# Performance work log

Hardware: AMD Instinct MI355X
Metric: run time of the kernel (lower is better)

Reference implementation:

```python
import jax, jax.numpy as jnp
import numpy as np

B, N, D = 2, 2048, 1024
CTX, TV = 256, 250
H, DH = 16, 64
INNER = H * DH          # 1024
FF = 4 * D              # 4096 (GEGLU inner)
SCALE = DH ** -0.5


def _layernorm(x, g, b):
    mu = x.mean(-1, keepdims=True)
    var = ((x - mu) ** 2).mean(-1, keepdims=True)
    return (x - mu) / jnp.sqrt(var + 1e-5) * g + b


def _attn(xq, ctx, wq, wk, wv, wo, bo):
    b, n, _ = xq.shape
    m = ctx.shape[1]
    q = (xq @ wq).reshape(b, n, H, DH)
    k = (ctx @ wk).reshape(b, m, H, DH)
    v = (ctx @ wv).reshape(b, m, H, DH)
    sim = jnp.einsum('bihd,bjhd->bhij', q, k) * SCALE
    att = jax.nn.softmax(sim, axis=-1)
    out = jnp.einsum('bhij,bjhd->bihd', att, v).reshape(b, n, INNER)
    return out @ wo + bo


def _sin_pe(T, d):
    pos = jnp.arange(T, dtype=jnp.float32)[:, None]
    den = jnp.power(10000.0, 2.0 * jnp.arange(d // 2, dtype=jnp.float32) / d)
    ang = pos / den                                  # [T, d/2]
    return jnp.stack([jnp.sin(ang), jnp.cos(ang)], -1).reshape(T, d)


def setup_inputs() -> dict:
    key = jax.random.key(0)
    ks = jax.random.split(key, 40)
    w = lambda k, s: jax.random.normal(k, s, jnp.float32) * 0.02
    inp = {
        'x': jax.random.normal(ks[0], (B, N, D), jnp.float32),
        'context': jax.random.normal(ks[1], (B, CTX, D), jnp.float32),
        'hint_control': jax.random.normal(ks[2], (B, TV, D), jnp.float32),
        'ln1_g': jnp.ones((D,)), 'ln1_b': jnp.zeros((D,)),
        'ln2_g': jnp.ones((D,)), 'ln2_b': jnp.zeros((D,)),
        'ln3_g': jnp.ones((D,)), 'ln3_b': jnp.zeros((D,)),
        'ln4_g': jnp.ones((D,)), 'ln4_b': jnp.zeros((D,)),
        'a1_wq': w(ks[3], (D, INNER)), 'a1_wk': w(ks[4], (D, INNER)),
        'a1_wv': w(ks[5], (D, INNER)), 'a1_wo': w(ks[6], (INNER, D)),
        'a1_bo': jnp.zeros((D,)),
        'a2_wq': w(ks[7], (D, INNER)), 'a2_wk': w(ks[8], (D, INNER)),
        'a2_wv': w(ks[9], (D, INNER)), 'a2_wo': w(ks[10], (INNER, D)),
        'a2_bo': jnp.zeros((D,)),
        'a3_wq': w(ks[11], (D, INNER)), 'a3_wk': w(ks[12], (D, INNER)),
        'a3_wv': w(ks[13], (D, INNER)), 'a3_wo': w(ks[14], (INNER, D)),
        'a3_bo': jnp.zeros((D,)),
        'ff_w1': w(ks[15], (D, 2 * FF)), 'ff_b1': jnp.zeros((2 * FF,)),
        'ff_w2': w(ks[16], (FF, D)), 'ff_b2': jnp.zeros((D,)),
    }
    return inp


def reference(x, context, hint_control,
              ln1_g, ln1_b, ln2_g, ln2_b, ln3_g, ln3_b, ln4_g, ln4_b,
              a1_wq, a1_wk, a1_wv, a1_wo, a1_bo,
              a2_wq, a2_wk, a2_wv, a2_wo, a2_bo,
              a3_wq, a3_wk, a3_wv, a3_wo, a3_bo,
              ff_w1, ff_b1, ff_w2, ff_b2):
    # attn1: self-attention (disable_self_attn=False -> context is x itself)
    h = _layernorm(x, ln1_g, ln1_b)
    x = _attn(h, h, a1_wq, a1_wk, a1_wv, a1_wo, a1_bo) + x
    # attn2: cross-attention over context
    h = _layernorm(x, ln2_g, ln2_b)
    x = _attn(h, context, a2_wq, a2_wk, a2_wv, a2_wo, a2_bo) + x
    # attn3: video cross-attention with sinusoidal PE added to hint_control
    hint = hint_control + _sin_pe(hint_control.shape[1], D)[None]
    h = _layernorm(x, ln4_g, ln4_b)
    x = _attn(h, hint, a3_wq, a3_wk, a3_wv, a3_wo, a3_bo) + x
    # GEGLU feed-forward
    h = _layernorm(x, ln3_g, ln3_b)
    proj = h @ ff_w1 + ff_b1
    a, gate = jnp.split(proj, 2, axis=-1)
    x = (a * jax.nn.gelu(gate, approximate=False)) @ ff_w2 + ff_b2 + x
    return x
```

## Files before the change

kernel.cpp:

```cpp
#include <hip/hip_runtime.h>
#include <cstdint>

typedef unsigned short u16;
typedef __bf16 bf16x8 __attribute__((ext_vector_type(8)));
typedef float f32x4 __attribute__((ext_vector_type(4)));

__device__ __forceinline__ u16 f2bf(float f) {
  union { float f; uint32_t u; } x; x.f = f;
  uint32_t r = x.u + 0x7FFFu + ((x.u >> 16) & 1u);
  return (u16)(r >> 16);
}
__device__ __forceinline__ bf16x8 ld8s(const u16* p) {
  return *reinterpret_cast<const bf16x8*>(p);
}
__device__ __forceinline__ float geluf(float x) {
  return 0.5f * x * (1.f + erff(x * 0.70710678118654752f));
}
__device__ __forceinline__ uint32_t cvtpk(float a, float b) {
  uint32_t r;
  asm("v_cvt_pk_bf16_f32 %0, %1, %2" : "=v"(r) : "v"(a), "v"(b));
  return r;
}
__device__ __forceinline__ void gload16(const u16* g, u16* l) {
  __builtin_amdgcn_global_load_lds(
      (__attribute__((address_space(1))) void*)const_cast<u16*>(g),
      (__attribute__((address_space(3))) void*)l, 16, 0, 0);
}

struct PrepJob {
  const void* src; void* dst;
  int K, N, mode, row_off, ldo, s_lo, s_hi, blk0;
};
struct PrepArgs { PrepJob j[17]; };

__global__ __launch_bounds__(256) void wprep_kernel(PrepArgs a) {
  __shared__ float tile[32][33];
  int bid = blockIdx.x;
  int t = threadIdx.x;
  const float* src = nullptr; void* dst = nullptr;
  int K = 0, N = 0, mode = 0, roff = 0, ldo = 0, slo = 0, shi = 0, bl = 0;
#pragma unroll
  for (int i = 0; i < 17; ++i) {
    int lo = a.j[i].blk0;
    int hi = (i == 16) ? 0x7fffffff : a.j[i + 1].blk0;
    if (bid >= lo && bid < hi) {
      src = (const float*)a.j[i].src; dst = a.j[i].dst;
      K = a.j[i].K; N = a.j[i].N; mode = a.j[i].mode; roff = a.j[i].row_off;
      ldo = a.j[i].ldo; slo = a.j[i].s_lo; shi = a.j[i].s_hi; bl = bid - lo;
    }
  }
  (void)K;
  if (mode <= 1) {
    int nb = N >> 5;
    int bx = bl % nb, by = bl / nb;
    int tx = t & 31, ty = t >> 5;
    int n = bx * 32 + tx, kbase = by * 32;
#pragma unroll
    for (int r = 0; r < 4; ++r)
      tile[ty + r * 8][tx] = src[(size_t)(kbase + ty + r * 8) * N + n];
    __syncthreads();
#pragma unroll
    for (int r = 0; r < 4; ++r) {
      int nl = ty + r * 8, ng = bx * 32 + nl;
      int orow;
      if (mode == 0) orow = roff + ng;
      else {
        if (ng < 4096) orow = ((ng >> 4) << 5) + (ng & 15);
        else { int t2 = ng - 4096; orow = ((t2 >> 4) << 5) + 16 + (t2 & 15); }
      }
      float v = tile[tx][nl];
      if (mode == 0 && orow >= slo && orow < shi) v *= 0.18033688011112042f;
      ((u16*)dst)[(size_t)orow * ldo + kbase + tx] = f2bf(v);
    }
  } else if (mode == 2) {
    int idx = bl * 1024 + t * 4;
    float4 v = *reinterpret_cast<const float4*>(src + idx);
    ushort4 o;
    o.x = f2bf(v.x); o.y = f2bf(v.y); o.z = f2bf(v.z); o.w = f2bf(v.w);
    *reinterpret_cast<ushort4*>((u16*)dst + idx) = o;
  } else if (mode == 3) {
    int row = bl;
    int tt = row % 250;
    int d0 = t * 4;
    int i0 = d0 >> 1;
    float den0 = powf(10000.f, (float)i0 / 512.f);
    float den1 = powf(10000.f, (float)(i0 + 1) / 512.f);
    float a0 = (float)tt / den0, a1 = (float)tt / den1;
    const float* hp = src + (size_t)row * 1024 + d0;
    u16* op = (u16*)dst + (size_t)row * 1024 + d0;
    op[0] = f2bf(hp[0] + sinf(a0));
    op[1] = f2bf(hp[1] + cosf(a0));
    op[2] = f2bf(hp[2] + sinf(a1));
    op[3] = f2bf(hp[3] + cosf(a1));
  } else {
    int i2 = bl * 256 + t;
    int g = i2 >> 5, s2 = i2 & 31;
    int c2 = (s2 < 16) ? (g * 16 + s2) : (4096 + g * 16 + (s2 - 16));
    ((float*)dst)[i2] = src[c2];
  }
}

__global__ __launch_bounds__(256) void ln_kernel(const float* __restrict__ x,
                                                 const float* __restrict__ g,
                                                 const float* __restrict__ b,
                                                 u16* __restrict__ out) {
  int row = blockIdx.x;
  int tid = threadIdx.x;
  int l = tid & 63, w = tid >> 6;
  const float4 v = reinterpret_cast<const float4*>(x + (size_t)row * 1024)[tid];
  float s = v.x + v.y + v.z + v.w;
#pragma unroll
  for (int d = 1; d < 64; d <<= 1) s += __shfl_xor(s, d, 64);
  __shared__ float red[8];
  if (l == 0) red[w] = s;
  __syncthreads();
  float mean = (red[0] + red[1] + red[2] + red[3]) * (1.f / 1024.f);
  float dx = v.x - mean, dy = v.y - mean, dz = v.z - mean, dw = v.w - mean;
  float vs = dx * dx + dy * dy + dz * dz + dw * dw;
#pragma unroll
  for (int d = 1; d < 64; d <<= 1) vs += __shfl_xor(vs, d, 64);
  if (l == 0) red[4 + w] = vs;
  __syncthreads();
  float var = (red[4] + red[5] + red[6] + red[7]) * (1.f / 1024.f);
  float rstd = rsqrtf(var + 1e-5f);
  const float4 g4 = reinterpret_cast<const float4*>(g)[tid];
  const float4 b4 = reinterpret_cast<const float4*>(b)[tid];
  ushort4 o;
  o.x = f2bf(dx * rstd * g4.x + b4.x);
  o.y = f2bf(dy * rstd * g4.y + b4.y);
  o.z = f2bf(dz * rstd * g4.z + b4.z);
  o.w = f2bf(dw * rstd * g4.w + b4.w);
  reinterpret_cast<ushort4*>(out + (size_t)row * 1024)[tid] = o;
}

template <int EPI>
__global__ __launch_bounds__(512, 2) void gemm256_kernel(
    const u16* __restrict__ A, int lda, const u16* __restrict__ Bt,
    void* __restrict__ Cv, int ldc, const float* __restrict__ bias,
    int M, int N, int K) {
  __shared__ __align__(16) u16 As[2][256 * 64];
  __shared__ __align__(16) u16 Bs[2][256 * 64];
  int t = threadIdx.x;
  int l = t & 63, w = t >> 6;
  int wm = w >> 2, wn = w & 3;
  int lr = l & 15, lg = l >> 4;
  int gx = gridDim.x;
  int nwg = gx * gridDim.y;
  int orig = blockIdx.y * gx + blockIdx.x;
  int qq = nwg >> 3, rr = nwg & 7;
  int xcd = orig & 7, lin = orig >> 3;
  int wg = (xcd < rr ? xcd * (qq + 1) : rr * (qq + 1) + (xcd - rr) * qq) + lin;
  int bx = wg % gx, by = wg / gx;
  int row0 = by * 256, n0 = bx * 256;

  int lrow8 = l >> 3, lchunk = l & 7;
  int csrc = (lchunk ^ lrow8) * 8;
  int keyA = lr & 15 & 7;
  int c0 = ((lg ^ keyA) << 3);
  int c1 = (((4 + lg) ^ keyA) << 3);

  f32x4 acc[8][4];
#pragma unroll
  for (int i = 0; i < 8; ++i)
#pragma unroll
    for (int j = 0; j < 4; ++j) acc[i][j] = f32x4{0.f, 0.f, 0.f, 0.f};

  auto stA = [&](int buf, int k0, int q) {
    int rb = q * 64 + w * 8;
    gload16(&A[(size_t)(row0 + rb + lrow8) * lda + k0 + csrc], &As[buf][rb * 64]);
  };
  auto stB = [&](int buf, int k0, int q) {
    int rb = q * 64 + w * 8;
    gload16(&Bt[(size_t)(n0 + rb + lrow8) * K + k0 + csrc], &Bs[buf][rb * 64]);
  };

  int nk = K >> 6;
  stB(0, 0, 0); stB(0, 0, 1); stB(0, 0, 2); stB(0, 0, 3);
  stA(0, 0, 0); stA(0, 0, 2); stA(0, 0, 1); stA(0, 0, 3);
  asm volatile("s_waitcnt vmcnt(2)" ::: "memory");
  __builtin_amdgcn_sched_barrier(0);
  asm volatile("s_barrier" ::: "memory");

  for (int ti = 0; ti < nk; ++ti) {
    int cur = ti & 1, nxt = cur ^ 1;
    bool hn = (ti + 1 < nk);
    int k0n = (ti + 1) << 6;
    const u16* Ab = As[cur];
    const u16* Bb = Bs[cur];
    bf16x8 a[4], b[4];

#pragma unroll
    for (int mi = 0; mi < 4; ++mi) a[mi] = ld8s(&Ab[(wm * 128 + mi * 16 + lr) * 64 + c0]);
#pragma unroll
    for (int ni = 0; ni < 4; ++ni) b[ni] = ld8s(&Bb[(wn * 64 + ni * 16 + lr) * 64 + c0]);
    if (hn) { stB(nxt, k0n, 0); stB(nxt, k0n, 1); }
    asm volatile("s_barrier" ::: "memory");
    __builtin_amdgcn_s_setprio(1);
#pragma unroll
    for (int mi = 0; mi < 4; ++mi)
#pragma unroll
      for (int ni = 0; ni < 4; ++ni)
        acc[mi][ni] = __builtin_amdgcn_mfma_f32_16x16x32_bf16(a[mi], b[ni], acc[mi][ni], 0, 0, 0);
    __builtin_amdgcn_s_setprio(0);
    if (hn) asm volatile("s_waitcnt vmcnt(2)" ::: "memory");
    else    asm volatile("s_waitcnt vmcnt(0)" ::: "memory");
    __builtin_amdgcn_sched_barrier(0);
    asm volatile("s_barrier" ::: "memory");

#pragma unroll
    for (int mi = 0; mi < 4; ++mi) a[mi] = ld8s(&Ab[(wm * 128 + (mi + 4) * 16 + lr) * 64 + c0]);
    if (hn) { stB(nxt, k0n, 2); stB(nxt, k0n, 3); }
    asm volatile("s_barrier" ::: "memory");
    __builtin_amdgcn_s_setprio(1);
#pragma unroll
    for (int mi = 0; mi < 4; ++mi)
#pragma unroll
      for (int ni = 0; ni < 4; ++ni)
        acc[mi + 4][ni] = __builtin_amdgcn_mfma_f32_16x16x32_bf16(a[mi], b[ni], acc[mi + 4][ni], 0, 0, 0);
    __builtin_amdgcn_s_setprio(0);
    asm volatile("s_barrier" ::: "memory");

#pragma unroll
    for (int mi = 0; mi < 4; ++mi) a[mi] = ld8s(&Ab[(wm * 128 + mi * 16 + lr) * 64 + c1]);
#pragma unroll
    for (int ni = 0; ni < 4; ++ni) b[ni] = ld8s(&Bb[(wn * 64 + ni * 16 + lr) * 64 + c1]);
    if (hn) { stA(nxt, k0n, 0); stA(nxt, k0n, 2); }
    asm volatile("s_barrier" ::: "memory");
    __builtin_amdgcn_s_setprio(1);
#pragma unroll
    for (int mi = 0; mi < 4; ++mi)
#pragma unroll
      for (int ni = 0; ni < 4; ++ni)
        acc[mi][ni] = __builtin_amdgcn_mfma_f32_16x16x32_bf16(a[mi], b[ni], acc[mi][ni], 0, 0, 0);
    __builtin_amdgcn_s_setprio(0);
    asm volatile("s_barrier" ::: "memory");

#pragma unroll
    for (int mi = 0; mi < 4; ++mi) a[mi] = ld8s(&Ab[(wm * 128 + (mi + 4) * 16 + lr) * 64 + c1]);
    if (hn) { stA(nxt, k0n, 1); stA(nxt, k0n, 3); }
    asm volatile("s_barrier" ::: "memory");
    __builtin_amdgcn_s_setprio(1);
#pragma unroll
    for (int mi = 0; mi < 4; ++mi)
#pragma unroll
      for (int ni = 0; ni < 4; ++ni)
        acc[mi + 4][ni] = __builtin_amdgcn_mfma_f32_16x16x32_bf16(a[mi], b[ni], acc[mi + 4][ni], 0, 0, 0);
    __builtin_amdgcn_s_setprio(0);
    if (hn) asm volatile("s_waitcnt vmcnt(2)" ::: "memory");
    __builtin_amdgcn_sched_barrier(0);
    asm volatile("s_barrier" ::: "memory");
  }

#pragma unroll
  for (int mi = 0; mi < 8; ++mi) {
    int rowb = row0 + wm * 128 + mi * 16 + lg * 4;
    if (EPI == 2) {
#pragma unroll
      for (int p = 0; p < 2; ++p) {
        int colA = n0 + wn * 64 + p * 32 + lr;
        int colG = colA + 16;
        int ocol = ((n0 + wn * 64) >> 1) + p * 16 + lr;
#pragma unroll
        for (int r = 0; r < 4; ++r) {
          float av = acc[mi][2 * p][r] + bias[colA];
          float gv = acc[mi][2 * p + 1][r] + bias[colG];
          ((u16*)Cv)[(size_t)(rowb + r) * ldc + ocol] = f2bf(av * geluf(gv));
        }
      }
    } else {
#pragma unroll
      for (int ni = 0; ni < 4; ++ni) {
        int gcol = n0 + wn * 64 + ni * 16 + lr;
#pragma unroll
        for (int r = 0; r < 4; ++r)
          ((u16*)Cv)[(size_t)(rowb + r) * ldc + gcol] = f2bf(acc[mi][ni][r]);
      }
    }
  }
}

template <int EPI, bool GUARD>
__global__ __launch_bounds__(256) void gemm_bt_kernel(
    const u16* __restrict__ A, int lda, const u16* __restrict__ Bt,
    void* __restrict__ Cv, int ldc, const float* __restrict__ bias,
    const float* __restrict__ res, int M, int N, int K) {
  __shared__ __align__(16) u16 As[2][128 * 64];
  __shared__ __align__(16) u16 Bs[2][128 * 64];
  int t = threadIdx.x;
  int l = t & 63, w = t >> 6;
  int wm = w >> 1, wn = w & 1;
  int lr = l & 15, lg = l >> 4;
  int gx = gridDim.x;
  int nwg = gx * gridDim.y;
  int orig = blockIdx.y * gx + blockIdx.x;
  int qq = nwg >> 3, rr = nwg & 7;
  int xcd = orig & 7, lin = orig >> 3;
  int wg = (xcd < rr ? xcd * (qq + 1) : rr * (qq + 1) + (xcd - rr) * qq) + lin;
  int bx = wg % gx, by = wg / gx;
  int row0 = by * 128, n0 = bx * 128;

  int lrow8 = l >> 3, lchunk = l & 7;
  int csrc = (lchunk ^ lrow8) * 8;
  int keyA = lr & 7;
  f32x4 acc[4][4];
#pragma unroll
  for (int i = 0; i < 4; ++i)
#pragma unroll
    for (int j = 0; j < 4; ++j) acc[i][j] = f32x4{0.f, 0.f, 0.f, 0.f};

  auto stage = [&](int buf, int k0) {
#pragma unroll
    for (int q = 0; q < 4; ++q) {
      int rbase = w * 32 + q * 8;
      int r = rbase + lrow8;
      int ga = row0 + r;
      if (GUARD) { if (ga > M - 1) ga = M - 1; }
      gload16(&A[(size_t)ga * lda + k0 + csrc], &As[buf][rbase * 64]);
      gload16(&Bt[(size_t)(n0 + r) * K + k0 + csrc], &Bs[buf][rbase * 64]);
    }
  };

  int nk = K >> 6;
  stage(0, 0);
  if (nk > 1) {
    stage(1, 64);
    asm volatile("s_waitcnt vmcnt(8)" ::: "memory");
  } else {
    asm volatile("s_waitcnt vmcnt(0)" ::: "memory");
  }
  __builtin_amdgcn_sched_barrier(0);
  __builtin_amdgcn_s_barrier();
  int cur = 0;
  for (int ti = 0; ti < nk; ++ti) {
    __builtin_amdgcn_s_setprio(1);
#pragma unroll
    for (int kk = 0; kk < 2; ++kk) {
      bf16x8 af[4], bfv[4];
#pragma unroll
      for (int mi = 0; mi < 4; ++mi)
        af[mi] = ld8s(&As[cur][(wm * 64 + mi * 16 + lr) * 64 + ((((kk << 2) + lg) ^ keyA) << 3)]);
#pragma unroll
      for (int ni = 0; ni < 4; ++ni)
        bfv[ni] = ld8s(&Bs[cur][(wn * 64 + ni * 16 + lr) * 64 + ((((kk << 2) + lg) ^ keyA) << 3)]);
#pragma unroll
      for (int mi = 0; mi < 4; ++mi)
#pragma unroll
        for (int ni = 0; ni < 4; ++ni)
          acc[mi][ni] = __builtin_amdgcn_mfma_f32_16x16x32_bf16(af[mi], bfv[ni], acc[mi][ni], 0, 0, 0);
    }
    __builtin_amdgcn_s_setprio(0);
    __builtin_amdgcn_sched_barrier(0);
    __builtin_amdgcn_s_barrier();
    if (ti + 2 < nk) {
      stage(cur, (ti + 2) << 6);
      asm volatile("s_waitcnt vmcnt(8)" ::: "memory");
    } else {
      asm volatile("s_waitcnt vmcnt(0)" ::: "memory");
    }
    __builtin_amdgcn_sched_barrier(0);
    __builtin_amdgcn_s_barrier();
    cur ^= 1;
  }

#pragma unroll
  for (int mi = 0; mi < 4; ++mi) {
    int rowb = row0 + wm * 64 + mi * 16 + lg * 4;
    if (EPI == 2) {
#pragma unroll
      for (int p = 0; p < 2; ++p) {
        int colA = n0 + wn * 64 + p * 32 + lr;
        int colG = colA + 16;
        int ocol = ((n0 + wn * 64) >> 1) + p * 16 + lr;
#pragma unroll
        for (int r = 0; r < 4; ++r) {
          int grow = rowb + r;
          float av = acc[mi][2 * p][r] + bias[colA];
          float gv = acc[mi][2 * p + 1][r] + bias[colG];
          ((u16*)Cv)[(size_t)grow * ldc + ocol] = f2bf(av * geluf(gv));
        }
      }
    } else {
#pragma unroll
      for (int ni = 0; ni < 4; ++ni) {
        int gcol = n0 + wn * 64 + ni * 16 + lr;
#pragma unroll
        for (int r = 0; r < 4; ++r) {
          int grow = rowb + r;
          if (GUARD && grow >= M) continue;
          float v = acc[mi][ni][r];
          if (EPI == 0)
            ((u16*)Cv)[(size_t)grow * ldc + gcol] = f2bf(v);
          else
            ((float*)Cv)[(size_t)grow * ldc + gcol] =
                v + bias[gcol] + res[(size_t)grow * ldc + gcol];
        }
      }
    }
  }
}

template <bool TG>
__global__ __launch_bounds__(256) void attn_kernel(
    const u16* __restrict__ Q, int qs, int qoff,
    const u16* __restrict__ KV, int kvs, int koff, int voff,
    int m, u16* __restrict__ O) {
  int b = blockIdx.z, h = blockIdx.y;
  int t = threadIdx.x;
  int l = t & 63, w = t >> 6;
  int lr = l & 15, lg = l >> 4;
  int q0 = blockIdx.x * 128 + w * 16;
  __shared__ __align__(16) u16 Ks[2][64 * 64];
  __shared__ __align__(16) u16 Vt[2][64 * 64];
  __shared__ __align__(16) u16 Pl[4][16 * 64];

  const u16* qrowA = Q + (size_t)((b << 11) + q0 + lr) * qs + qoff + h * 64;
  const u16* qrowB = qrowA + (size_t)64 * qs;
  bf16x8 qa0 = ld8s(qrowA + lg * 8), qa1 = ld8s(qrowA + 32 + lg * 8);
  bf16x8 qb0 = ld8s(qrowB + lg * 8), qb1 = ld8s(qrowB + 32 + lg * 8);

  f32x4 oA[4], oB[4];
  float psA = 0.f, psB = 0.f;
#pragma unroll
  for (int r = 0; r < 4; ++r) { oA[r] = f32x4{0.f, 0.f, 0.f, 0.f}; oB[r] = f32x4{0.f, 0.f, 0.f, 0.f}; }

  const u16* kvb = KV + (size_t)b * m * kvs + h * 64;
  int kj = t >> 3, kc = t & 7;
  int srcsw = ((l & 7) ^ (l >> 3)) << 3;
  int psw = (lr & 7) ^ ((lr & 8) >> 1);

  {
#pragma unroll
    for (int q2 = 0; q2 < 2; ++q2) {
      int gr = w * 16 + q2 * 8 + (l >> 3);
      if (TG) { if (gr > m - 1) gr = m - 1; }
      gload16(kvb + (size_t)gr * kvs + koff + srcsw, &Ks[0][(w * 16 + q2 * 8) * 64]);
    }
    int jv = kj * 2;
    int gv0 = jv, gv1 = jv + 1;
    if (TG) { if (gv0 > m - 1) gv0 = m - 1; if (gv1 > m - 1) gv1 = m - 1; }
    uint4 va = *reinterpret_cast<const uint4*>(kvb + (size_t)gv0 * kvs + voff + kc * 8);
    uint4 vb2 = *reinterpret_cast<const uint4*>(kvb + (size_t)gv1 * kvs + voff + kc * 8);
    const u16* vap = reinterpret_cast<const u16*>(&va);
    const u16* vbp = reinterpret_cast<const u16*>(&vb2);
    int jb = jv >> 3, jlow = jv & 7;
#pragma unroll
    for (int i = 0; i < 8; ++i) {
      int d = kc * 8 + i;
      int key = (d ^ (d >> 3)) & 7;
      uint32_t pk = (uint32_t)vap[i] | ((uint32_t)vbp[i] << 16);
      *reinterpret_cast<uint32_t*>(&Vt[0][d * 64 + ((jb ^ key) << 3) + jlow]) = pk;
    }
  }
  __syncthreads();

  int nj = (m + 63) >> 6;
  int cur = 0;
  for (int jt = 0; jt < nj; ++jt) {
    int j0 = jt << 6;
    bool hn = (jt + 1 < nj);
    uint4 va, vb2;
    if (hn) {
      int j0n = j0 + 64;
#pragma unroll
      for (int q2 = 0; q2 < 2; ++q2) {
        int gr = j0n + w * 16 + q2 * 8 + (l >> 3);
        if (TG) { if (gr > m - 1) gr = m - 1; }
        gload16(kvb + (size_t)gr * kvs + koff + srcsw, &Ks[cur ^ 1][(w * 16 + q2 * 8) * 64]);
      }
      int jv = kj * 2;
      int gv0 = j0n + jv, gv1 = j0n + jv + 1;
      if (TG) { if (gv0 > m - 1) gv0 = m - 1; if (gv1 > m - 1) gv1 = m - 1; }
      va = *reinterpret_cast<const uint4*>(kvb + (size_t)gv0 * kvs + voff + kc * 8);
      vb2 = *reinterpret_cast<const uint4*>(kvb + (size_t)gv1 * kvs + voff + kc * 8);
    }

    const u16* Kb = Ks[cur];
    f32x4 sA[4], sB[4];
#pragma unroll
    for (int c = 0; c < 4; ++c) {
      sA[c] = f32x4{0.f, 0.f, 0.f, 0.f};
      sB[c] = f32x4{0.f, 0.f, 0.f, 0.f};
      bf16x8 k0 = ld8s(&Kb[(c * 16 + lr) * 64 + ((lg ^ (lr & 7)) << 3)]);
      bf16x8 k1 = ld8s(&Kb[(c * 16 + lr) * 64 + (((4 + lg) ^ (lr & 7)) << 3)]);
      sA[c] = __builtin_amdgcn_mfma_f32_16x16x32_bf16(k0, qa0, sA[c], 0, 0, 0);
      sA[c] = __builtin_amdgcn_mfma_f32_16x16x32_bf16(k1, qa1, sA[c], 0, 0, 0);
      sB[c] = __builtin_amdgcn_mfma_f32_16x16x32_bf16(k0, qb0, sB[c], 0, 0, 0);
      sB[c] = __builtin_amdgcn_mfma_f32_16x16x32_bf16(k1, qb1, sB[c], 0, 0, 0);
    }

    if (hn) {
      const u16* vap = reinterpret_cast<const u16*>(&va);
      const u16* vbp = reinterpret_cast<const u16*>(&vb2);
      int jv = kj * 2;
      int jb = jv >> 3, jlow = jv & 7;
#pragma unroll
      for (int i = 0; i < 8; ++i) {
        int d = kc * 8 + i;
        int key = (d ^ (d >> 3)) & 7;
        uint32_t pk = (uint32_t)vap[i] | ((uint32_t)vbp[i] << 16);
        *reinterpret_cast<uint32_t*>(&Vt[cur ^ 1][d * 64 + ((jb ^ key) << 3) + jlow]) = pk;
      }
    }

    bool tail = TG && (j0 + 64 > m);
    const u16* Vb = Vt[cur];
    bf16x8 vfr[2][4];

    {
      uint32_t pk[8];
#pragma unroll
      for (int c = 0; c < 4; ++c) {
        float p[4];
#pragma unroll
        for (int r = 0; r < 4; ++r) {
          float v = exp2f(sA[c][r]);
          if (tail && (j0 + c * 16 + lg * 4 + r >= m)) v = 0.f;
          p[r] = v; psA += v;
        }
        pk[2 * c] = cvtpk(p[0], p[1]);
        pk[2 * c + 1] = cvtpk(p[2], p[3]);
      }
#pragma unroll
      for (int c = 0; c < 4; ++c) {
        int phys = (2 * c + (lg >> 1)) ^ psw;
        uint2 u; u.x = pk[2 * c]; u.y = pk[2 * c + 1];
        *reinterpret_cast<uint2*>(&Pl[w][lr * 64 + (phys << 3) + ((lg & 1) << 2)]) = u;
      }
#pragma unroll
      for (int ks = 0; ks < 2; ++ks) {
        int physp = (ks * 4 + lg) ^ psw;
        bf16x8 pb = ld8s(&Pl[w][lr * 64 + (physp << 3)]);
#pragma unroll
        for (int dt = 0; dt < 4; ++dt) {
          int d = dt * 16 + lr;
          int key = (d ^ (d >> 3)) & 7;
          vfr[ks][dt] = ld8s(&Vb[d * 64 + ((((ks << 2) + lg) ^ key) << 3)]);
          oA[dt] = __builtin_amdgcn_mfma_f32_16x16x32_bf16(vfr[ks][dt], pb, oA[dt], 0, 0, 0);
        }
      }
    }
    {
      uint32_t pk[8];
#pragma unroll
      for (int c = 0; c < 4; ++c) {
        float p[4];
#pragma unroll
        for (int r = 0; r < 4; ++r) {
          float v = exp2f(sB[c][r]);
          if (tail && (j0 + c * 16 + lg * 4 + r >= m)) v = 0.f;
          p[r] = v; psB += v;
        }
        pk[2 * c] = cvtpk(p[0], p[1]);
        pk[2 * c + 1] = cvtpk(p[2], p[3]);
      }
#pragma unroll
      for (int c = 0; c < 4; ++c) {
        int phys = (2 * c + (lg >> 1)) ^ psw;
        uint2 u; u.x = pk[2 * c]; u.y = pk[2 * c + 1];
        *reinterpret_cast<uint2*>(&Pl[w][lr * 64 + (phys << 3) + ((lg & 1) << 2)]) = u;
      }
#pragma unroll
      for (int ks = 0; ks < 2; ++ks) {
        int physp = (ks * 4 + lg) ^ psw;
        bf16x8 pb = ld8s(&Pl[w][lr * 64 + (physp << 3)]);
#pragma unroll
        for (int dt = 0; dt < 4; ++dt)
          oB[dt] = __builtin_amdgcn_mfma_f32_16x16x32_bf16(vfr[ks][dt], pb, oB[dt], 0, 0, 0);
      }
    }
    __syncthreads();
    cur ^= 1;
  }

  psA += __shfl_xor(psA, 16, 64); psA += __shfl_xor(psA, 32, 64);
  psB += __shfl_xor(psB, 16, 64); psB += __shfl_xor(psB, 32, 64);
  float invA = 1.f / psA, invB = 1.f / psB;
  {
    int grow = (b << 11) + q0 + lr;
    u16* op = O + (size_t)grow * 1024 + h * 64 + lg * 4;
#pragma unroll
    for (int dt = 0; dt < 4; ++dt) {
      uint2 u;
      u.x = cvtpk(oA[dt][0] * invA, oA[dt][1] * invA);
      u.y = cvtpk(oA[dt][2] * invA, oA[dt][3] * invA);
      *reinterpret_cast<uint2*>(op + dt * 16) = u;
    }
    u16* op2 = op + (size_t)64 * 1024;
#pragma unroll
    for (int dt = 0; dt < 4; ++dt) {
      uint2 u;
      u.x = cvtpk(oB[dt][0] * invB, oB[dt][1] * invB);
      u.y = cvtpk(oB[dt][2] * invB, oB[dt][3] * invB);
      *reinterpret_cast<uint2*>(op2 + dt * 16) = u;
    }
  }
}

extern "C" void kernel_launch(void* const* d_in, const int* in_sizes, int n_in,
                              void* d_out, int out_size, void* d_ws, size_t ws_size,
                              hipStream_t stream) {
  const float* x_in = (const float*)d_in[0];
  const float* ctx_in = (const float*)d_in[1];
  const float* hint_in = (const float*)d_in[2];
  const float* ln1g = (const float*)d_in[3]; const float* ln1b = (const float*)d_in[4];
  const float* ln2g = (const float*)d_in[5]; const float* ln2b = (const float*)d_in[6];
  const float* ln3g = (const float*)d_in[7]; const float* ln3b = (const float*)d_in[8];
  const float* ln4g = (const float*)d_in[9]; const float* ln4b = (const float*)d_in[10];
  const float* a1wq = (const float*)d_in[11]; const float* a1wk = (const float*)d_in[12];
  const float* a1wv = (const float*)d_in[13]; const float* a1wo = (const float*)d_in[14];
  const float* a1bo = (const float*)d_in[15];
  const float* a2wq = (const float*)d_in[16]; const float* a2wk = (const float*)d_in[17];
  const float* a2wv = (const float*)d_in[18]; const float* a2wo = (const float*)d_in[19];
  const float* a2bo = (const float*)d_in[20];
  const float* a3wq = (const float*)d_in[21]; const float* a3wk = (const float*)d_in[22];
  const float* a3wv = (const float*)d_in[23]; const float* a3wo = (const float*)d_in[24];
  const float* a3bo = (const float*)d_in[25];
  const float* ffw1 = (const float*)d_in[26]; const float* ffb1 = (const float*)d_in[27];
  const float* ffw2 = (const float*)d_in[28]; const float* ffb2 = (const float*)d_in[29];

  char* wsb = (char*)d_ws;
  size_t off = 0;
  auto alloc = [&](size_t bytes) -> void* {
    void* p = wsb + off;
    off += (bytes + 255) & ~(size_t)255;
    return p;
  };
  u16* wqkv1t = (u16*)alloc(3072ull * 1024 * 2);
  u16* wo1t = (u16*)alloc(1024ull * 1024 * 2);
  u16* wq2t = (u16*)alloc(1024ull * 1024 * 2);
  u16* wkv2t = (u16*)alloc(2048ull * 1024 * 2);
  u16* wo2t = (u16*)alloc(1024ull * 1024 * 2);
  u16* wq3t = (u16*)alloc(1024ull * 1024 * 2);
  u16* wkv3t = (u16*)alloc(2048ull * 1024 * 2);
  u16* wo3t = (u16*)alloc(1024ull * 1024 * 2);
  u16* w1t = (u16*)alloc(8192ull * 1024 * 2);
  u16* w2t = (u16*)alloc(1024ull * 4096 * 2);
  float* b1p = (float*)alloc(8192ull * 4);
  u16* hintbf = (u16*)alloc(500ull * 1024 * 2);
  u16* ctxbf = (u16*)alloc(512ull * 1024 * 2);
  float* xbuf = (float*)alloc(4096ull * 1024 * 4);
  u16* hbf = (u16*)alloc(4096ull * 1024 * 2);
  u16* attnout = (u16*)alloc(4096ull * 1024 * 2);
  u16* qbuf = (u16*)alloc(4096ull * 1024 * 2);
  u16* kvbuf = (u16*)alloc(512ull * 2048 * 2);
  u16* qkv = (u16*)alloc(4096ull * 4096 * 2);
  u16* gbuf = qkv;

  PrepArgs pa;
  int bi = 0, bc = 0;
  auto addJ = [&](const void* s, void* d, int K, int N, int mode, int roff,
                  int ldo, int slo, int shi, int nblk) {
    pa.j[bi].src = s; pa.j[bi].dst = d; pa.j[bi].K = K; pa.j[bi].N = N;
    pa.j[bi].mode = mode; pa.j[bi].row_off = roff; pa.j[bi].ldo = ldo;
    pa.j[bi].s_lo = slo; pa.j[bi].s_hi = shi; pa.j[bi].blk0 = bc;
    bc += nblk; ++bi;
  };
  addJ(a1wq, wqkv1t, 1024, 1024, 0, 0, 1024, 0, 1024, 1024);
  addJ(a1wk, wqkv1t, 1024, 1024, 0, 1024, 1024, 0, 0, 1024);
  addJ(a1wv, wqkv1t, 1024, 1024, 0, 2048, 1024, 0, 0, 1024);
  addJ(a1wo, wo1t, 1024, 1024, 0, 0, 1024, 0, 0, 1024);
  addJ(a2wq, wq2t, 1024, 1024, 0, 0, 1024, 0, 1024, 1024);
  addJ(a2wk, wkv2t, 1024, 1024, 0, 0, 1024, 0, 0, 1024);
  addJ(a2wv, wkv2t, 1024, 1024, 0, 1024, 1024, 0, 0, 1024);
  addJ(a2wo, wo2t, 1024, 1024, 0, 0, 1024, 0, 0, 1024);
  addJ(a3wq, wq3t, 1024, 1024, 0, 0, 1024, 0, 1024, 1024);
  addJ(a3wk, wkv3t, 1024, 1024, 0, 0, 1024, 0, 0, 1024);
  addJ(a3wv, wkv3t, 1024, 1024, 0, 1024, 1024, 0, 0, 1024);
  addJ(a3wo, wo3t, 1024, 1024, 0, 0, 1024, 0, 0, 1024);
  addJ(ffw1, w1t, 1024, 8192, 1, 0, 1024, 0, 0, 8192);
  addJ(ffw2, w2t, 4096, 1024, 0, 0, 4096, 0, 0, 4096);
  addJ(ctx_in, ctxbf, 0, 0, 2, 0, 0, 0, 0, 512);
  addJ(hint_in, hintbf, 0, 0, 3, 0, 0, 0, 0, 500);
  addJ(ffb1, b1p, 0, 0, 4, 0, 0, 0, 0, 32);
  wprep_kernel<<<bc, 256, 0, stream>>>(pa);

  ln_kernel<<<4096, 256, 0, stream>>>(x_in, ln1g, ln1b, hbf);
  gemm256_kernel<0><<<dim3(12, 16), 512, 0, stream>>>(hbf, 1024, wqkv1t, qkv, 3072,
                                                      nullptr, 4096, 3072, 1024);
  attn_kernel<false><<<dim3(16, 16, 2), 256, 0, stream>>>(qkv, 3072, 0, qkv, 3072, 1024, 2048,
                                                          2048, attnout);
  gemm_bt_kernel<1, false><<<dim3(8, 32), 256, 0, stream>>>(attnout, 1024, wo1t, xbuf, 1024,
                                                            a1bo, x_in, 4096, 1024, 1024);

  ln_kernel<<<4096, 256, 0, stream>>>(xbuf, ln2g, ln2b, hbf);
  gemm_bt_kernel<0, false><<<dim3(8, 32), 256, 0, stream>>>(hbf, 1024, wq2t, qbuf, 1024,
                                                            nullptr, nullptr, 4096, 1024, 1024);
  gemm_bt_kernel<0, false><<<dim3(16, 4), 256, 0, stream>>>(ctxbf, 1024, wkv2t, kvbuf, 2048,
                                                            nullptr, nullptr, 512, 2048, 1024);
  attn_kernel<false><<<dim3(16, 16, 2), 256, 0, stream>>>(qbuf, 1024, 0, kvbuf, 2048, 0, 1024,
                                                          256, attnout);
  gemm_bt_kernel<1, false><<<dim3(8, 32), 256, 0, stream>>>(attnout, 1024, wo2t, xbuf, 1024,
                                                            a2bo, xbuf, 4096, 1024, 1024);

  ln_kernel<<<4096, 256, 0, stream>>>(xbuf, ln4g, ln4b, hbf);
  gemm_bt_kernel<0, false><<<dim3(8, 32), 256, 0, stream>>>(hbf, 1024, wq3t, qbuf, 1024,
                                                            nullptr, nullptr, 4096, 1024, 1024);
  gemm_bt_kernel<0, true><<<dim3(16, 4), 256, 0, stream>>>(hintbf, 1024, wkv3t, kvbuf, 2048,
                                                           nullptr, nullptr, 500, 2048, 1024);
  attn_kernel<true><<<dim3(16, 16, 2), 256, 0, stream>>>(qbuf, 1024, 0, kvbuf, 2048, 0, 1024,
                                                         250, attnout);
  gemm_bt_kernel<1, false><<<dim3(8, 32), 256, 0, stream>>>(attnout, 1024, wo3t, xbuf, 1024,
                                                            a3bo, xbuf, 4096, 1024, 1024);

  ln_kernel<<<4096, 256, 0, stream>>>(xbuf, ln3g, ln3b, hbf);
  gemm256_kernel<2><<<dim3(32, 16), 512, 0, stream>>>(hbf, 1024, w1t, gbuf, 4096,
                                                      b1p, 4096, 8192, 1024);
  gemm_bt_kernel<1, false><<<dim3(8, 32), 256, 0, stream>>>(gbuf, 4096, w2t, d_out, 1024,
                                                            ffb2, xbuf, 4096, 1024, 4096);
}
```

Before: 499.1 us.

## Split self-attention KV range in two and reduce partial outputs

The self-attention launch now splits the 2048-key range into two halves across extra blocks. Each block writes an unnormalized bf16 partial output and its row sums, and a new reduction kernel adds the two partials and divides by the combined sum. The aim is to double the number of blocks, since 512 blocks leave the GPU under-occupied. The cost is an extra kernel launch, extra global traffic for the partials, and bf16 rounding of unnormalized partials. Combining halves by plain sums appears to rely on the kernel not using a per-split running max.

```diff
diff --git a/kernel.cpp b/kernel.cpp
--- a/kernel.cpp
+++ b/kernel.cpp
@@ -9,6 +9,9 @@
   union { float f; uint32_t u; } x; x.f = f;
   uint32_t r = x.u + 0x7FFFu + ((x.u >> 16) & 1u);
   return (u16)(r >> 16);
+}
+__device__ __forceinline__ float bf2f(u16 u) {
+  union { float f; uint32_t x; } v; v.x = (uint32_t)u << 16; return v.f;
 }
 __device__ __forceinline__ bf16x8 ld8s(const u16* p) {
   return *reinterpret_cast<const bf16x8*>(p);
@@ -133,6 +136,24 @@
   reinterpret_cast<ushort4*>(out + (size_t)row * 1024)[tid] = o;
 }
 
+__global__ __launch_bounds__(256) void attnred_kernel(
+    const u16* __restrict__ O0, const u16* __restrict__ O1,
+    const float* __restrict__ ps, u16* __restrict__ out) {
+  int row = blockIdx.x;
+  int c4 = threadIdx.x << 2;
+  int h = c4 >> 6;
+  float inv = 1.f / (ps[row * 16 + h] + ps[65536 + row * 16 + h]);
+  size_t idx = (size_t)row * 1024 + c4;
+  ushort4 a = *reinterpret_cast<const ushort4*>(O0 + idx);
+  ushort4 b = *reinterpret_cast<const ushort4*>(O1 + idx);
+  ushort4 o;
+  o.x = f2bf((bf2f(a.x) + bf2f(b.x)) * inv);
+  o.y = f2bf((bf2f(a.y) + bf2f(b.y)) * inv);
+  o.z = f2bf((bf2f(a.z) + bf2f(b.z)) * inv);
+  o.w = f2bf((bf2f(a.w) + bf2f(b.w)) * inv);
+  *reinterpret_cast<ushort4*>(out + idx) = o;
+}
+
 template <int EPI>
 __global__ __launch_bounds__(512, 2) void gemm256_kernel(
     const u16* __restrict__ A, int lda, const u16* __restrict__ Bt,
@@ -155,7 +176,7 @@
 
   int lrow8 = l >> 3, lchunk = l & 7;
   int csrc = (lchunk ^ lrow8) * 8;
-  int keyA = lr & 15 & 7;
+  int keyA = lr & 7;
   int c0 = ((lg ^ keyA) << 3);
   int c1 = (((4 + lg) ^ keyA) << 3);
 
@@ -399,12 +420,16 @@
   }
 }
 
-template <bool TG>
+template <bool TG, int OMODE>
 __global__ __launch_bounds__(256) void attn_kernel(
     const u16* __restrict__ Q, int qs, int qoff,
     const u16* __restrict__ KV, int kvs, int koff, int voff,
-    int m, u16* __restrict__ O) {
-  int b = blockIdx.z, h = blockIdx.y;
+    int m, int kvlen,
+    u16* __restrict__ O0, u16* __restrict__ O1, float* __restrict__ psout) {
+  int hf = (OMODE == 1) ? (blockIdx.z & 1) : 0;
+  int b = (OMODE == 1) ? (blockIdx.z >> 1) : blockIdx.z;
+  int kv0 = hf * kvlen;
+  int h = blockIdx.y;
   int t = threadIdx.x;
   int l = t & 63, w = t >> 6;
   int lr = l & 15, lg = l >> 4;
@@ -431,12 +456,12 @@
   {
 #pragma unroll
     for (int q2 = 0; q2 < 2; ++q2) {
-      int gr = w * 16 + q2 * 8 + (l >> 3);
+      int gr = kv0 + w * 16 + q2 * 8 + (l >> 3);
       if (TG) { if (gr > m - 1) gr = m - 1; }
       gload16(kvb + (size_t)gr * kvs + koff + srcsw, &Ks[0][(w * 16 + q2 * 8) * 64]);
     }
     int jv = kj * 2;
-    int gv0 = jv, gv1 = jv + 1;
+    int gv0 = kv0 + jv, gv1 = kv0 + jv + 1;
     if (TG) { if (gv0 > m - 1) gv0 = m - 1; if (gv1 > m - 1) gv1 = m - 1; }
     uint4 va = *reinterpret_cast<const uint4*>(kvb + (size_t)gv0 * kvs + voff + kc * 8);
     uint4 vb2 = *reinterpret_cast<const uint4*>(kvb + (size_t)gv1 * kvs + voff + kc * 8);
@@ -453,10 +478,10 @@
   }
   __syncthreads();
 
-  int nj = (m + 63) >> 6;
+  int nj = (kvlen + 63) >> 6;
   int cur = 0;
   for (int jt = 0; jt < nj; ++jt) {
-    int j0 = jt << 6;
+    int j0 = kv0 + (jt << 6);
     bool hn = (jt + 1 < nj);
     uint4 va, vb2;
     if (hn) {
@@ -574,10 +599,32 @@
 
   psA += __shfl_xor(psA, 16, 64); psA += __shfl_xor(psA, 32, 64);
   psB += __shfl_xor(psB, 16, 64); psB += __shfl_xor(psB, 32, 64);
-  float invA = 1.f / psA, invB = 1.f / psB;
-  {
-    int grow = (b << 11) + q0 + lr;
-    u16* op = O + (size_t)grow * 1024 + h * 64 + lg * 4;
+  int grow = (b << 11) + q0 + lr;
+  if (OMODE == 1) {
+    u16* Ob = hf ? O1 : O0;
+    u16* op = Ob + (size_t)grow * 1024 + h * 64 + lg * 4;
+#pragma unroll
+    for (int dt = 0; dt < 4; ++dt) {
+      uint2 u;
+      u.x = cvtpk(oA[dt][0], oA[dt][1]);
+      u.y = cvtpk(oA[dt][2], oA[dt][3]);
+      *reinterpret_cast<uint2*>(op + dt * 16) = u;
+    }
+    u16* op2 = op + (size_t)64 * 1024;
+#pragma unroll
+    for (int dt = 0; dt < 4; ++dt) {
+      uint2 u;
+      u.x = cvtpk(oB[dt][0], oB[dt][1]);
+      u.y = cvtpk(oB[dt][2], oB[dt][3]);
+      *reinterpret_cast<uint2*>(op2 + dt * 16) = u;
+    }
+    if (lg == 0) {
+      psout[hf * 65536 + grow * 16 + h] = psA;
+      psout[hf * 65536 + (grow + 64) * 16 + h] = psB;
+    }
+  } else {
+    float invA = 1.f / psA, invB = 1.f / psB;
+    u16* op = O0 + (size_t)grow * 1024 + h * 64 + lg * 4;
 #pragma unroll
     for (int dt = 0; dt < 4; ++dt) {
       uint2 u;
@@ -645,6 +692,7 @@
   u16* kvbuf = (u16*)alloc(512ull * 2048 * 2);
   u16* qkv = (u16*)alloc(4096ull * 4096 * 2);
   u16* gbuf = qkv;
+  float* psbuf = (float*)kvbuf;
 
   PrepArgs pa;
   int bi = 0, bc = 0;
@@ -677,9 +725,10 @@
   ln_kernel<<<4096, 256, 0, stream>>>(x_in, ln1g, ln1b, hbf);
   gemm256_kernel<0><<<dim3(12, 16), 512, 0, stream>>>(hbf, 1024, wqkv1t, qkv, 3072,
                                                       nullptr, 4096, 3072, 1024);
-  attn_kernel<false><<<dim3(16, 16, 2), 256, 0, stream>>>(qkv, 3072, 0, qkv, 3072, 1024, 2048,
-                                                          2048, attnout);
-  gemm_bt_kernel<1, false><<<dim3(8, 32), 256, 0, stream>>>(attnout, 1024, wo1t, xbuf, 1024,
+  attn_kernel<false, 1><<<dim3(16, 16, 4), 256, 0, stream>>>(
+      qkv, 3072, 0, qkv, 3072, 1024, 2048, 2048, 1024, attnout, qbuf, psbuf);
+  attnred_kernel<<<4096, 256, 0, stream>>>(attnout, qbuf, psbuf, hbf);
+  gemm_bt_kernel<1, false><<<dim3(8, 32), 256, 0, stream>>>(hbf, 1024, wo1t, xbuf, 1024,
                                                             a1bo, x_in, 4096, 1024, 1024);
 
   ln_kernel<<<4096, 256, 0, stream>>>(xbuf, ln2g, ln2b, hbf);
@@ -687,8 +736,8 @@
                                                             nullptr, nullptr, 4096, 1024, 1024);
   gemm_bt_kernel<0, false><<<dim3(16, 4), 256, 0, stream>>>(ctxbf, 1024, wkv2t, kvbuf, 2048,
                                                             nullptr, nullptr, 512, 2048, 1024);
-  attn_kernel<false><<<dim3(16, 16, 2), 256, 0, stream>>>(qbuf, 1024, 0, kvbuf, 2048, 0, 1024,
-                                                          256, attnout);
+  attn_kernel<false, 0><<<dim3(16, 16, 2), 256, 0, stream>>>(
+      qbuf, 1024, 0, kvbuf, 2048, 0, 1024, 256, 256, attnout, nullptr, nullptr);
   gemm_bt_kernel<1, false><<<dim3(8, 32), 256, 0, stream>>>(attnout, 1024, wo2t, xbuf, 1024,
                                                             a2bo, xbuf, 4096, 1024, 1024);
 
@@ -697,8 +746,8 @@
                                                             nullptr, nullptr, 4096, 1024, 1024);
   gemm_bt_kernel<0, true><<<dim3(16, 4), 256, 0, stream>>>(hintbf, 1024, wkv3t, kvbuf, 2048,
                                                            nullptr, nullptr, 500, 2048, 1024);
-  attn_kernel<true><<<dim3(16, 16, 2), 256, 0, stream>>>(qbuf, 1024, 0, kvbuf, 2048, 0, 1024,
-                                                         250, attnout);
+  attn_kernel<true, 0><<<dim3(16, 16, 2), 256, 0, stream>>>(
+      qbuf, 1024, 0, kvbuf, 2048, 0, 1024, 250, 250, attnout, nullptr, nullptr);
   gemm_bt_kernel<1, false><<<dim3(8, 32), 256, 0, stream>>>(attnout, 1024, wo3t, xbuf, 1024,
                                                             a3bo, xbuf, 4096, 1024, 1024);
 
```

Result: no change. 508.2 us (+1.8%).
